# Performance work log

Measured on AMD Instinct MI355X. Metric: run time of the kernel, lower is better.

The kernel has to match this reference:

```python
import jax, jax.numpy as jnp
import numpy as np

N_CELLS = 200_000
N_FACES = 400_000
N_POINTS = 200_000
E_CF = 800_000
E_FP = 800_000
E_PP = 1_200_000
IN_C, IN_F, HID, OUT = 8, 8, 64, 128


def setup_inputs() -> dict:
    key = jax.random.key(0)
    ks = jax.random.split(key, 18)
    return {
        "x_centers": jax.random.normal(ks[0], (N_CELLS, IN_C), jnp.float32),
        "x_face": jax.random.normal(ks[1], (N_FACES, IN_F), jnp.float32),
        "W_cf": jax.random.normal(ks[2], (IN_C, HID), jnp.float32) * 0.1,
        "b_cf": jax.random.normal(ks[3], (HID,), jnp.float32) * 0.1,
        "W_fp": jax.random.normal(ks[4], (HID + IN_F, OUT), jnp.float32) * 0.1,
        "b_fp": jax.random.normal(ks[5], (OUT,), jnp.float32) * 0.1,
        "W_pp": jax.random.normal(ks[6], (OUT, OUT), jnp.float32) * 0.1,
        "W_pp_root": jax.random.normal(ks[7], (OUT, OUT), jnp.float32) * 0.1,
        "b_pp": jax.random.normal(ks[8], (OUT,), jnp.float32) * 0.1,
        "ea_cf": jax.random.uniform(ks[9], (E_CF,), jnp.float32),
        "ea_fp": jax.random.uniform(ks[10], (E_FP,), jnp.float32),
        "ea_pp": jax.random.uniform(ks[11], (E_PP,), jnp.float32),
        "src_cf": jax.random.randint(ks[12], (E_CF,), 0, N_CELLS, jnp.int32),
        "dst_cf": jax.random.randint(ks[13], (E_CF,), 0, N_FACES, jnp.int32),
        "src_fp": jax.random.randint(ks[14], (E_FP,), 0, N_FACES, jnp.int32),
        "dst_fp": jax.random.randint(ks[15], (E_FP,), 0, N_POINTS, jnp.int32),
        "src_pp": jax.random.randint(ks[16], (E_PP,), 0, N_POINTS, jnp.int32),
        "dst_pp": jax.random.randint(ks[17], (E_PP,), 0, N_POINTS, jnp.int32),
    }


def _graph_conv(x, W, b, src, dst, ea, n_dst):
    # transform-then-gather (small in-dim GEMM first), weight by edge_attr, scatter-sum
    h = x @ W                                   # [n_src, out]
    msg = h[src] * ea[:, None]                  # [E, out]
    return jax.ops.segment_sum(msg, dst, num_segments=n_dst) + b


def reference(x_centers, x_face, W_cf, b_cf, W_fp, b_fp, W_pp, W_pp_root, b_pp,
              ea_cf, ea_fp, ea_pp, src_cf, dst_cf, src_fp, dst_fp, src_pp, dst_pp):
    # layerCenterFace: cells -> faces
    y_face = _graph_conv(x_centers, W_cf, b_cf, src_cf, dst_cf, ea_cf, N_FACES)
    # concat learned face features with raw face features
    x = jnp.concatenate([y_face, x_face], axis=-1)          # [N_FACES, 72]
    # layerFacePoint: faces -> points
    y_pt = _graph_conv(x, W_fp, b_fp, src_fp, dst_fp, ea_fp, N_POINTS)
    # layerPointPoint: points -> points with root/self term
    msg = (y_pt @ W_pp)[src_pp] * ea_pp[:, None]            # [E_PP, 128]
    agg = jax.ops.segment_sum(msg, dst_pp, num_segments=N_POINTS)
    return y_pt @ W_pp_root + agg + b_pp                    # [N_POINTS, 128]
```

## Files before the change

kernel.cpp:

```cpp
#include <hip/hip_runtime.h>
#include <hip/hip_bf16.h>

#define N_CELLS  200000
#define N_FACES  400000
#define N_POINTS 200000
#define E_CF     800000
#define E_FP     800000
#define E_PP     1200000
#define CAP_CF   16
#define CAP_FP   24
#define CAP_PP   32
#define OVF_CAP  4096

typedef __attribute__((ext_vector_type(4))) float f32x4;

__device__ __forceinline__ int2 ldnt2(const int2* p) {
    long long v = __builtin_nontemporal_load((const long long*)p);
    int2 r; r.x = (int)(v & 0xffffffffLL); r.y = (int)(v >> 32); return r;
}

__device__ __forceinline__ void fill_fixed(const int* __restrict__ src,
                                           const int* __restrict__ dst,
                                           const float* __restrict__ ea,
                                           int nE, int rlo, int rhi, int cap,
                                           int tid0, int stride,
                                           int* __restrict__ cnt,
                                           int2* __restrict__ pe,
                                           int* __restrict__ ovfn,
                                           int4* __restrict__ ovf) {
    for (int e = tid0; e < nE; e += stride) {
        int4 d4 = *(const int4*)(dst + e);
        int4 s4 = *(const int4*)(src + e);
        float4 w4 = *(const float4*)(ea + e);
        int dd[4] = {d4.x, d4.y, d4.z, d4.w};
        int ss[4] = {s4.x, s4.y, s4.z, s4.w};
        float ww[4] = {w4.x, w4.y, w4.z, w4.w};
#pragma unroll
        for (int i = 0; i < 4; ++i) {
            int d = dd[i];
            if (d >= rlo && d < rhi) {
                int t = atomicAdd(&cnt[d], 1);
                if (t < cap)
                    pe[(size_t)d * cap + t] = make_int2(ss[i], __float_as_int(ww[i]));
                else {
                    int g = atomicAdd(ovfn, 1);
                    if (g < OVF_CAP) ovf[g] = make_int4(d, ss[i], __float_as_int(ww[i]), 0);
                }
            }
        }
    }
}

__global__ __launch_bounds__(256) void k_fillA(const int* __restrict__ src_cf,
                                               const int* __restrict__ dst_cf,
                                               const float* __restrict__ ea_cf,
                                               int* __restrict__ cnt_cf,
                                               int2* __restrict__ pe_cf,
                                               const int* __restrict__ src_fp,
                                               const int* __restrict__ dst_fp,
                                               const float* __restrict__ ea_fp,
                                               int* __restrict__ cnt_fp,
                                               int2* __restrict__ pe_fp,
                                               int* __restrict__ ovfn,
                                               int4* __restrict__ ovf_cf,
                                               int4* __restrict__ ovf_fp,
                                               const float* __restrict__ W_cf,
                                               const float* __restrict__ b_cf,
                                               const float* __restrict__ W_fp,
                                               const float* __restrict__ b_fp,
                                               const float* __restrict__ W_rt,
                                               const float* __restrict__ W_pp,
                                               const float* __restrict__ b_pp,
                                               float* __restrict__ WALL) {
    __shared__ float WcfS[512];
    __shared__ float bcfS[64];
    __shared__ float WtL[18 * 128];
    int b = blockIdx.x;
    if (b < 512) {
        int p = b & 3;
        int blk = b >> 2;
        int rlo = p * 100000, rhi = rlo + 100000;
        int tid0 = (blk * 256 + (int)threadIdx.x) * 4;
        fill_fixed(src_cf, dst_cf, ea_cf, E_CF, rlo, rhi, CAP_CF,
                   tid0, 128 * 256 * 4, cnt_cf, pe_cf, ovfn, ovf_cf);
    } else if (b < 1024) {
        int bb = b - 512;
        int p = bb & 3;
        int blk = bb >> 2;
        int rlo = p * 50000, rhi = rlo + 50000;
        int tid0 = (blk * 256 + (int)threadIdx.x) * 4;
        fill_fixed(src_fp, dst_fp, ea_fp, E_FP, rlo, rhi, CAP_FP,
                   tid0, 128 * 256 * 4, cnt_fp, pe_fp, ovfn + 1, ovf_fp);
    } else {
        for (int i = threadIdx.x; i < 512; i += 256) WcfS[i] = W_cf[i];
        if (threadIdx.x < 64) bcfS[threadIdx.x] = b_cf[threadIdx.x];
        __syncthreads();
        int t = threadIdx.x;
        int j = t & 127;
        if (t < 128) {
            float accW[8] = {};
            float accb = 0.f;
            for (int m = 0; m < 64; ++m) {
                float wf = W_fp[m * 128 + j];
#pragma unroll
                for (int k = 0; k < 8; ++k) accW[k] += WcfS[k * 64 + m] * wf;
                accb += bcfS[m] * wf;
            }
#pragma unroll
            for (int k = 0; k < 8; ++k) WtL[k * 128 + j] = accW[k];
            WtL[16 * 128 + j] = accb;
        } else {
#pragma unroll
            for (int k = 0; k < 8; ++k) WtL[(8 + k) * 128 + j] = W_fp[(64 + k) * 128 + j];
            WtL[17 * 128 + j] = b_fp[j];
        }
        __syncthreads();
        for (int i = threadIdx.x; i < 36 * 128; i += 256) {
            int r = i >> 7, jj = i & 127;
            float acc;
            if (r < 17) {
                acc = 0.f;
                for (int k = 0; k < 128; ++k) acc += WtL[r * 128 + k] * W_rt[k * 128 + jj];
            } else if (r < 34) {
                acc = 0.f;
                for (int k = 0; k < 128; ++k) acc += WtL[(r - 17) * 128 + k] * W_pp[k * 128 + jj];
            } else if (r == 34) {
                acc = 0.f;
                for (int k = 0; k < 128; ++k) acc += WtL[17 * 128 + k] * W_pp[k * 128 + jj];
            } else {
                acc = b_pp[jj];
                for (int k = 0; k < 128; ++k) acc += WtL[17 * 128 + k] * W_rt[k * 128 + jj];
            }
            WALL[i] = acc;
        }
    }
}

__global__ __launch_bounds__(256) void k_fillB(const int* __restrict__ src_pp,
                                               const int* __restrict__ dst_pp,
                                               const float* __restrict__ ea_pp,
                                               int* __restrict__ cnt_pp,
                                               int2* __restrict__ pe_pp,
                                               int* __restrict__ ovfn,
                                               int4* __restrict__ ovf_pp,
                                               const float* __restrict__ xc,
                                               const int* __restrict__ cnt_cf,
                                               const int2* __restrict__ pe_cf,
                                               const int* __restrict__ ovfn_cf,
                                               const int4* __restrict__ ovf_cf,
                                               const float* __restrict__ x_face,
                                               float* __restrict__ aggcx) {
    int b = blockIdx.x;
    if (b < 512) {
        int p = b & 3;
        int blk = b >> 2;
        int rlo = p * 50000, rhi = rlo + 50000;
        int tid0 = (blk * 256 + (int)threadIdx.x) * 4;
        fill_fixed(src_pp, dst_pp, ea_pp, E_PP, rlo, rhi, CAP_PP,
                   tid0, 128 * 256 * 4, cnt_pp, pe_pp, ovfn + 2, ovf_pp);
        return;
    }
    int r = (b - 512) * 256 + threadIdx.x;
    if (r >= N_FACES) return;
    int n = cnt_cf[r]; if (n > CAP_CF) n = CAP_CF;
    const int2* prow = pe_cf + (size_t)r * CAP_CF;
    float a[8] = {};
    int e = 0;
    for (; e + 1 < n; e += 2) {
        int2 q0 = prow[e], q1 = prow[e + 1];
        float w0 = __int_as_float(q0.y), w1 = __int_as_float(q1.y);
        const float* p0 = xc + (size_t)q0.x * 8;
        const float* p1 = xc + (size_t)q1.x * 8;
        float4 u0 = *(const float4*)p0, u1 = *(const float4*)(p0 + 4);
        float4 v0 = *(const float4*)p1, v1 = *(const float4*)(p1 + 4);
        a[0] += w0 * u0.x + w1 * v0.x; a[1] += w0 * u0.y + w1 * v0.y;
        a[2] += w0 * u0.z + w1 * v0.z; a[3] += w0 * u0.w + w1 * v0.w;
        a[4] += w0 * u1.x + w1 * v1.x; a[5] += w0 * u1.y + w1 * v1.y;
        a[6] += w0 * u1.z + w1 * v1.z; a[7] += w0 * u1.w + w1 * v1.w;
    }
    if (e < n) {
        int2 q0 = prow[e];
        float w0 = __int_as_float(q0.y);
        const float* p0 = xc + (size_t)q0.x * 8;
        float4 u0 = *(const float4*)p0, u1 = *(const float4*)(p0 + 4);
        a[0] += w0 * u0.x; a[1] += w0 * u0.y; a[2] += w0 * u0.z; a[3] += w0 * u0.w;
        a[4] += w0 * u1.x; a[5] += w0 * u1.y; a[6] += w0 * u1.z; a[7] += w0 * u1.w;
    }
    int no = *ovfn_cf;
    if (no > 0) {
        if (no > OVF_CAP) no = OVF_CAP;
        for (int i = 0; i < no; ++i) {
            int4 o = ovf_cf[i];
            if (o.x == r) {
                float w0 = __int_as_float(o.z);
                const float* p0 = xc + (size_t)o.y * 8;
#pragma unroll
                for (int k = 0; k < 8; ++k) a[k] += w0 * p0[k];
            }
        }
    }
    float4 xf0 = *(const float4*)(x_face + (size_t)r * 8);
    float4 xf1 = *(const float4*)(x_face + (size_t)r * 8 + 4);
    float4* o4 = (float4*)(aggcx + (size_t)r * 16);
    o4[0] = make_float4(a[0], a[1], a[2], a[3]);
    o4[1] = make_float4(a[4], a[5], a[6], a[7]);
    o4[2] = xf0;
    o4[3] = xf1;
}

__global__ __launch_bounds__(256) void k_g16(const float* __restrict__ aggcx,
                                             const int* __restrict__ cnt,
                                             const int2* __restrict__ pe,
                                             const int* __restrict__ ovfn,
                                             const int4* __restrict__ ovf,
                                             float* __restrict__ a16,
                                             float* __restrict__ s_fp) {
    const int grp = threadIdx.x >> 4;
    const int l = threadIdx.x & 15;
    const int row = blockIdx.x * 16 + grp;
    int n = cnt[row]; if (n > CAP_FP) n = CAP_FP;
    const int2* prow = pe + (size_t)row * CAP_FP;
    float acc = 0.f, s = 0.f;
    int e = 0;
    for (; e + 1 < n; e += 2) {
        int2 q0 = ldnt2(prow + e);
        int2 q1 = ldnt2(prow + e + 1);
        float w0 = __int_as_float(q0.y), w1 = __int_as_float(q1.y);
        acc += w0 * aggcx[(size_t)q0.x * 16 + l] + w1 * aggcx[(size_t)q1.x * 16 + l];
        s += w0 + w1;
    }
    if (e < n) {
        int2 q0 = ldnt2(prow + e);
        float w0 = __int_as_float(q0.y);
        acc += w0 * aggcx[(size_t)q0.x * 16 + l];
        s += w0;
    }
    int no = *ovfn;
    if (no > 0) {
        if (no > OVF_CAP) no = OVF_CAP;
        for (int i = 0; i < no; ++i) {
            int4 o = ovf[i];
            if (o.x == row) {
                float w0 = __int_as_float(o.z);
                acc += w0 * aggcx[(size_t)o.y * 16 + l];
                s += w0;
            }
        }
    }
    a16[(size_t)row * 16 + l] = acc;
    if (l == 0) s_fp[row] = s;
}

__global__ __launch_bounds__(256) void k_fin(const float* __restrict__ a16,
                                             const float* __restrict__ s_fp,
                                             const int* __restrict__ cnt,
                                             const int2* __restrict__ pe,
                                             const int* __restrict__ ovfn,
                                             const int4* __restrict__ ovf,
                                             const float* __restrict__ WALL,
                                             float* __restrict__ out) {
    __shared__ float W36[36 * 128];
    for (int i = threadIdx.x; i < 36 * 128; i += 256) W36[i] = WALL[i];
    __syncthreads();
    const int grp = threadIdx.x >> 4;
    const int l = threadIdx.x & 15;
    const int row = blockIdx.x * 16 + grp;
    int n = cnt[row]; if (n > CAP_PP) n = CAP_PP;
    const int2* prow = pe + (size_t)row * CAP_PP;
    float App = 0.f, Spp = 0.f, Tpp = 0.f;
    int e = 0;
    for (; e + 1 < n; e += 2) {
        int2 q0 = ldnt2(prow + e);
        int2 q1 = ldnt2(prow + e + 1);
        float w0 = __int_as_float(q0.y), w1 = __int_as_float(q1.y);
        App += w0 * a16[(size_t)q0.x * 16 + l] + w1 * a16[(size_t)q1.x * 16 + l];
        Spp += w0 * s_fp[q0.x] + w1 * s_fp[q1.x];
        Tpp += w0 + w1;
    }
    if (e < n) {
        int2 q0 = ldnt2(prow + e);
        float w0 = __int_as_float(q0.y);
        App += w0 * a16[(size_t)q0.x * 16 + l];
        Spp += w0 * s_fp[q0.x];
        Tpp += w0;
    }
    int no = *ovfn;
    if (no > 0) {
        if (no > OVF_CAP) no = OVF_CAP;
        for (int i = 0; i < no; ++i) {
            int4 o = ovf[i];
            if (o.x == row) {
                float w0 = __int_as_float(o.z);
                App += w0 * a16[(size_t)o.y * 16 + l];
                Spp += w0 * s_fp[o.y];
                Tpp += w0;
            }
        }
    }
    float aown = a16[(size_t)row * 16 + l];
    float sown = s_fp[row];
    const int jc = l * 8;
    float o[8];
    {
        const float4* bb = (const float4*)(W36 + 35 * 128 + jc);
        const float4* sr = (const float4*)(W36 + 16 * 128 + jc);
        const float4* Sr = (const float4*)(W36 + 33 * 128 + jc);
        const float4* Tr = (const float4*)(W36 + 34 * 128 + jc);
        float4 b0 = bb[0], b1 = bb[1];
        float4 s0 = sr[0], s1 = sr[1];
        float4 S0 = Sr[0], S1 = Sr[1];
        float4 T0 = Tr[0], T1 = Tr[1];
        o[0] = b0.x + sown * s0.x + Spp * S0.x + Tpp * T0.x;
        o[1] = b0.y + sown * s0.y + Spp * S0.y + Tpp * T0.y;
        o[2] = b0.z + sown * s0.z + Spp * S0.z + Tpp * T0.z;
        o[3] = b0.w + sown * s0.w + Spp * S0.w + Tpp * T0.w;
        o[4] = b1.x + sown * s1.x + Spp * S1.x + Tpp * T1.x;
        o[5] = b1.y + sown * s1.y + Spp * S1.y + Tpp * T1.y;
        o[6] = b1.z + sown * s1.z + Spp * S1.z + Tpp * T1.z;
        o[7] = b1.w + sown * s1.w + Spp * S1.w + Tpp * T1.w;
    }
#pragma unroll
    for (int r = 0; r < 16; ++r) {
        float av = __shfl(aown, r, 16);
        const float4* wr = (const float4*)(W36 + r * 128 + jc);
        float4 w0 = wr[0], w1 = wr[1];
        o[0] += av * w0.x; o[1] += av * w0.y; o[2] += av * w0.z; o[3] += av * w0.w;
        o[4] += av * w1.x; o[5] += av * w1.y; o[6] += av * w1.z; o[7] += av * w1.w;
    }
#pragma unroll
    for (int r = 0; r < 16; ++r) {
        float av = __shfl(App, r, 16);
        const float4* wr = (const float4*)(W36 + (17 + r) * 128 + jc);
        float4 w0 = wr[0], w1 = wr[1];
        o[0] += av * w0.x; o[1] += av * w0.y; o[2] += av * w0.z; o[3] += av * w0.w;
        o[4] += av * w1.x; o[5] += av * w1.y; o[6] += av * w1.z; o[7] += av * w1.w;
    }
    float* op = out + (size_t)row * 128 + jc;
    f32x4 v0 = {o[0], o[1], o[2], o[3]};
    f32x4 v1 = {o[4], o[5], o[6], o[7]};
    __builtin_nontemporal_store(v0, (f32x4*)op);
    __builtin_nontemporal_store(v1, (f32x4*)(op + 4));
}

extern "C" void kernel_launch(void* const* d_in, const int* in_sizes, int n_in,
                              void* d_out, int out_size, void* d_ws, size_t ws_size,
                              hipStream_t stream) {
    const float* x_centers = (const float*)d_in[0];
    const float* x_face    = (const float*)d_in[1];
    const float* W_cf      = (const float*)d_in[2];
    const float* b_cf      = (const float*)d_in[3];
    const float* W_fp      = (const float*)d_in[4];
    const float* b_fp      = (const float*)d_in[5];
    const float* W_pp      = (const float*)d_in[6];
    const float* W_rt      = (const float*)d_in[7];
    const float* b_pp      = (const float*)d_in[8];
    const float* ea_cf     = (const float*)d_in[9];
    const float* ea_fp     = (const float*)d_in[10];
    const float* ea_pp     = (const float*)d_in[11];
    const int* src_cf      = (const int*)d_in[12];
    const int* dst_cf      = (const int*)d_in[13];
    const int* src_fp      = (const int*)d_in[14];
    const int* dst_fp      = (const int*)d_in[15];
    const int* src_pp      = (const int*)d_in[16];
    const int* dst_pp      = (const int*)d_in[17];
    float* out = (float*)d_out;

    char* ws = (char*)d_ws;
    float* aggcx           = (float*)(ws + 0);
    float* a16             = (float*)(ws + 28000000);
    float* s_fp            = (float*)(ws + 42000000);
    float* WALL            = (float*)(ws + 44000000);
    int2* pe_fp            = (int2*)(ws + 50000000);
    int2* pe_cf            = (int2*)(ws + 90000000);
    int2* pe_pp            = (int2*)(ws + 145000000);
    int*  cnt_cf           = (int*)(ws + 280000000);
    int*  cnt_fp           = (int*)(ws + 281600000);
    int*  cnt_pp           = (int*)(ws + 282400000);
    int*  ovfn             = (int*)(ws + 283200000);
    int4* ovf_cf           = (int4*)(ws + 284000000);
    int4* ovf_fp           = (int4*)(ws + 284100000);
    int4* ovf_pp           = (int4*)(ws + 284200000);

    (void)hipMemsetAsync(cnt_cf, 0, 3200016, stream);
    k_fillA<<<1025, 256, 0, stream>>>(src_cf, dst_cf, ea_cf, cnt_cf, pe_cf,
                                      src_fp, dst_fp, ea_fp, cnt_fp, pe_fp,
                                      ovfn, ovf_cf, ovf_fp,
                                      W_cf, b_cf, W_fp, b_fp, W_rt, W_pp, b_pp,
                                      WALL);
    k_fillB<<<512 + 1563, 256, 0, stream>>>(src_pp, dst_pp, ea_pp, cnt_pp, pe_pp,
                                            ovfn, ovf_pp,
                                            x_centers, cnt_cf, pe_cf, ovfn, ovf_cf,
                                            x_face, aggcx);
    k_g16<<<12500, 256, 0, stream>>>(aggcx, cnt_fp, pe_fp, ovfn + 1, ovf_fp, a16, s_fp);
    k_fin<<<12500, 256, 0, stream>>>(a16, s_fp, cnt_pp, pe_pp, ovfn + 2, ovf_pp, WALL, out);
}
```

Baseline: 342.0 us.

## Store a16 intermediate in bf16 and swap fp/pp CSR fills between kernels

The 16-wide intermediate a16 is now written as bf16 and read back as bf16 in the final gather, halving the bytes per random gather over E_PP edges. The point-point edge bucketing moves into the first fill kernel and the face-point bucketing into the second. This places the pp fill early and the fp fill right before its consumer, which may rebalance the work between the two launches. The bf16 storage adds rounding error to the aggregated features.

Result: faster. 333.9 us (-2.4%).

```diff
diff --git a/kernel.cpp b/kernel.cpp
--- a/kernel.cpp
+++ b/kernel.cpp
@@ -14,6 +14,13 @@
 
 typedef __attribute__((ext_vector_type(4))) float f32x4;
 
+__device__ __forceinline__ float bf2f(unsigned short u) {
+    union { unsigned int i; float f; } v; v.i = ((unsigned int)u) << 16; return v.f;
+}
+__device__ __forceinline__ unsigned short f2bf(float f) {
+    __hip_bfloat16 h = __float2bfloat16(f);
+    return *reinterpret_cast<unsigned short*>(&h);
+}
 __device__ __forceinline__ int2 ldnt2(const int2* p) {
     long long v = __builtin_nontemporal_load((const long long*)p);
     int2 r; r.x = (int)(v & 0xffffffffLL); r.y = (int)(v >> 32); return r;
@@ -56,14 +63,14 @@
                                                const float* __restrict__ ea_cf,
                                                int* __restrict__ cnt_cf,
                                                int2* __restrict__ pe_cf,
-                                               const int* __restrict__ src_fp,
-                                               const int* __restrict__ dst_fp,
-                                               const float* __restrict__ ea_fp,
-                                               int* __restrict__ cnt_fp,
-                                               int2* __restrict__ pe_fp,
+                                               const int* __restrict__ src_pp,
+                                               const int* __restrict__ dst_pp,
+                                               const float* __restrict__ ea_pp,
+                                               int* __restrict__ cnt_pp,
+                                               int2* __restrict__ pe_pp,
                                                int* __restrict__ ovfn,
                                                int4* __restrict__ ovf_cf,
-                                               int4* __restrict__ ovf_fp,
+                                               int4* __restrict__ ovf_pp,
                                                const float* __restrict__ W_cf,
                                                const float* __restrict__ b_cf,
                                                const float* __restrict__ W_fp,
@@ -89,8 +96,8 @@
         int blk = bb >> 2;
         int rlo = p * 50000, rhi = rlo + 50000;
         int tid0 = (blk * 256 + (int)threadIdx.x) * 4;
-        fill_fixed(src_fp, dst_fp, ea_fp, E_FP, rlo, rhi, CAP_FP,
-                   tid0, 128 * 256 * 4, cnt_fp, pe_fp, ovfn + 1, ovf_fp);
+        fill_fixed(src_pp, dst_pp, ea_pp, E_PP, rlo, rhi, CAP_PP,
+                   tid0, 128 * 256 * 4, cnt_pp, pe_pp, ovfn + 2, ovf_pp);
     } else {
         for (int i = threadIdx.x; i < 512; i += 256) WcfS[i] = W_cf[i];
         if (threadIdx.x < 64) bcfS[threadIdx.x] = b_cf[threadIdx.x];
@@ -136,13 +143,13 @@
     }
 }
 
-__global__ __launch_bounds__(256) void k_fillB(const int* __restrict__ src_pp,
-                                               const int* __restrict__ dst_pp,
-                                               const float* __restrict__ ea_pp,
-                                               int* __restrict__ cnt_pp,
-                                               int2* __restrict__ pe_pp,
+__global__ __launch_bounds__(256) void k_fillB(const int* __restrict__ src_fp,
+                                               const int* __restrict__ dst_fp,
+                                               const float* __restrict__ ea_fp,
+                                               int* __restrict__ cnt_fp,
+                                               int2* __restrict__ pe_fp,
                                                int* __restrict__ ovfn,
-                                               int4* __restrict__ ovf_pp,
+                                               int4* __restrict__ ovf_fp,
                                                const float* __restrict__ xc,
                                                const int* __restrict__ cnt_cf,
                                                const int2* __restrict__ pe_cf,
@@ -156,8 +163,8 @@
         int blk = b >> 2;
         int rlo = p * 50000, rhi = rlo + 50000;
         int tid0 = (blk * 256 + (int)threadIdx.x) * 4;
-        fill_fixed(src_pp, dst_pp, ea_pp, E_PP, rlo, rhi, CAP_PP,
-                   tid0, 128 * 256 * 4, cnt_pp, pe_pp, ovfn + 2, ovf_pp);
+        fill_fixed(src_fp, dst_fp, ea_fp, E_FP, rlo, rhi, CAP_FP,
+                   tid0, 128 * 256 * 4, cnt_fp, pe_fp, ovfn + 1, ovf_fp);
         return;
     }
     int r = (b - 512) * 256 + threadIdx.x;
@@ -213,7 +220,7 @@
                                              const int2* __restrict__ pe,
                                              const int* __restrict__ ovfn,
                                              const int4* __restrict__ ovf,
-                                             float* __restrict__ a16,
+                                             unsigned short* __restrict__ a16b,
                                              float* __restrict__ s_fp) {
     const int grp = threadIdx.x >> 4;
     const int l = threadIdx.x & 15;
@@ -247,11 +254,11 @@
             }
         }
     }
-    a16[(size_t)row * 16 + l] = acc;
+    a16b[(size_t)row * 16 + l] = f2bf(acc);
     if (l == 0) s_fp[row] = s;
 }
 
-__global__ __launch_bounds__(256) void k_fin(const float* __restrict__ a16,
+__global__ __launch_bounds__(256) void k_fin(const unsigned short* __restrict__ a16b,
                                              const float* __restrict__ s_fp,
                                              const int* __restrict__ cnt,
                                              const int2* __restrict__ pe,
@@ -273,14 +280,14 @@
         int2 q0 = ldnt2(prow + e);
         int2 q1 = ldnt2(prow + e + 1);
         float w0 = __int_as_float(q0.y), w1 = __int_as_float(q1.y);
-        App += w0 * a16[(size_t)q0.x * 16 + l] + w1 * a16[(size_t)q1.x * 16 + l];
+        App += w0 * bf2f(a16b[(size_t)q0.x * 16 + l]) + w1 * bf2f(a16b[(size_t)q1.x * 16 + l]);
         Spp += w0 * s_fp[q0.x] + w1 * s_fp[q1.x];
         Tpp += w0 + w1;
     }
     if (e < n) {
         int2 q0 = ldnt2(prow + e);
         float w0 = __int_as_float(q0.y);
-        App += w0 * a16[(size_t)q0.x * 16 + l];
+        App += w0 * bf2f(a16b[(size_t)q0.x * 16 + l]);
         Spp += w0 * s_fp[q0.x];
         Tpp += w0;
     }
@@ -291,13 +298,13 @@
             int4 o = ovf[i];
             if (o.x == row) {
                 float w0 = __int_as_float(o.z);
-                App += w0 * a16[(size_t)o.y * 16 + l];
+                App += w0 * bf2f(a16b[(size_t)o.y * 16 + l]);
                 Spp += w0 * s_fp[o.y];
                 Tpp += w0;
             }
         }
     }
-    float aown = a16[(size_t)row * 16 + l];
+    float aown = bf2f(a16b[(size_t)row * 16 + l]);
     float sown = s_fp[row];
     const int jc = l * 8;
     float o[8];
@@ -367,8 +374,8 @@
 
     char* ws = (char*)d_ws;
     float* aggcx           = (float*)(ws + 0);
-    float* a16             = (float*)(ws + 28000000);
-    float* s_fp            = (float*)(ws + 42000000);
+    unsigned short* a16b   = (unsigned short*)(ws + 28000000);
+    float* s_fp            = (float*)(ws + 36000000);
     float* WALL            = (float*)(ws + 44000000);
     int2* pe_fp            = (int2*)(ws + 50000000);
     int2* pe_cf            = (int2*)(ws + 90000000);
@@ -383,14 +390,14 @@
 
     (void)hipMemsetAsync(cnt_cf, 0, 3200016, stream);
     k_fillA<<<1025, 256, 0, stream>>>(src_cf, dst_cf, ea_cf, cnt_cf, pe_cf,
-                                      src_fp, dst_fp, ea_fp, cnt_fp, pe_fp,
-                                      ovfn, ovf_cf, ovf_fp,
+                                      src_pp, dst_pp, ea_pp, cnt_pp, pe_pp,
+                                      ovfn, ovf_cf, ovf_pp,
                                       W_cf, b_cf, W_fp, b_fp, W_rt, W_pp, b_pp,
                                       WALL);
-    k_fillB<<<512 + 1563, 256, 0, stream>>>(src_pp, dst_pp, ea_pp, cnt_pp, pe_pp,
-                                            ovfn, ovf_pp,
+    k_fillB<<<512 + 1563, 256, 0, stream>>>(src_fp, dst_fp, ea_fp, cnt_fp, pe_fp,
+                                            ovfn, ovf_fp,
                                             x_centers, cnt_cf, pe_cf, ovfn, ovf_cf,
                                             x_face, aggcx);
-    k_g16<<<12500, 256, 0, stream>>>(aggcx, cnt_fp, pe_fp, ovfn + 1, ovf_fp, a16, s_fp);
-    k_fin<<<12500, 256, 0, stream>>>(a16, s_fp, cnt_pp, pe_pp, ovfn + 2, ovf_pp, WALL, out);
-}
+    k_g16<<<12500, 256, 0, stream>>>(aggcx, cnt_fp, pe_fp, ovfn + 1, ovf_fp, a16b, s_fp);
+    k_fin<<<12500, 256, 0, stream>>>(a16b, s_fp, cnt_pp, pe_pp, ovfn + 2, ovf_pp, WALL, out);
+}
```
